# Kernel optimization log

Measured on AMD Instinct MI355X. Metric: run time of the kernel, lower is better.

## Reference

```python
import jax, jax.numpy as jnp
import numpy as np

WS = 16       # window size
SHIFT = 8     # shift size
HEADS = 16
DIM = 512
HIDDEN = 2048
B, H, W = 8, 64, 64
EPS = 1e-5


def _rel_coords_table(ws):
    h = np.arange(-(ws - 1), ws, dtype=np.float32)
    t = np.stack(np.meshgrid(h, h, indexing='ij'), axis=-1)  # (2ws-1, 2ws-1, 2)
    t = t / (ws - 1) * 8.0
    t = np.sign(t) * np.log2(np.abs(t) + 1.0) / np.log2(8.0)
    return t.reshape(-1, 2)


def _rel_pos_index(ws):
    coords = np.stack(np.meshgrid(np.arange(ws), np.arange(ws), indexing='ij'))
    cf = coords.reshape(2, -1)                      # (2, N)
    rel = (cf[:, :, None] - cf[:, None, :]).transpose(1, 2, 0)  # (N, N, 2)
    rel[..., 0] += ws - 1
    rel[..., 1] += ws - 1
    rel[..., 0] *= 2 * ws - 1
    return rel.sum(-1)                              # (N, N)


def _attn_mask(h, w, ws, shift):
    img = np.zeros((h, w))
    cnt = 0
    for hs in (slice(0, -ws), slice(-ws, -shift), slice(-shift, None)):
        for wsl in (slice(0, -ws), slice(-ws, -shift), slice(-shift, None)):
            img[hs, wsl] = cnt
            cnt += 1
    mw = img.reshape(h // ws, ws, w // ws, ws).transpose(0, 2, 1, 3).reshape(-1, ws * ws)
    am = mw[:, None, :] - mw[:, :, None]            # (nW, N, N)
    return np.where(am != 0, -100.0, 0.0).astype(np.float32)


def _ln(x, g, b):
    m = x.mean(-1, keepdims=True)
    v = ((x - m) ** 2).mean(-1, keepdims=True)
    return (x - m) * jax.lax.rsqrt(v + EPS) * g + b


def setup_inputs() -> dict:
    key = jax.random.key(0)
    ks = jax.random.split(key, 16)
    s = 0.02
    return {
        'x': jax.random.normal(ks[0], (B, H, W, DIM), jnp.float32),
        'qkv_w': jax.random.normal(ks[1], (3 * DIM, DIM), jnp.float32) * s,
        'q_bias': jnp.zeros((DIM,), jnp.float32),
        'v_bias': jnp.zeros((DIM,), jnp.float32),
        'logit_scale': jnp.full((HEADS, 1, 1), np.log(10.0), jnp.float32),
        'cpb_w1': jax.random.normal(ks[2], (512, 2), jnp.float32) * s,
        'cpb_b1': jnp.zeros((512,), jnp.float32),
        'cpb_w2': jax.random.normal(ks[3], (HEADS, 512), jnp.float32) * s,
        'proj_w': jax.random.normal(ks[4], (DIM, DIM), jnp.float32) * s,
        'proj_b': jnp.zeros((DIM,), jnp.float32),
        'norm1_g': jnp.ones((DIM,), jnp.float32),
        'norm1_b': jnp.zeros((DIM,), jnp.float32),
        'norm2_g': jnp.ones((DIM,), jnp.float32),
        'norm2_b': jnp.zeros((DIM,), jnp.float32),
        'fc1_w': jax.random.normal(ks[5], (HIDDEN, DIM), jnp.float32) * s,
        'fc1_b': jnp.zeros((HIDDEN,), jnp.float32),
        'fc2_w': jax.random.normal(ks[6], (DIM, HIDDEN), jnp.float32) * s,
        'fc2_b': jnp.zeros((DIM,), jnp.float32),
    }


def reference(x, qkv_w, q_bias, v_bias, logit_scale, cpb_w1, cpb_b1, cpb_w2,
              proj_w, proj_b, norm1_g, norm1_b, norm2_g, norm2_b,
              fc1_w, fc1_b, fc2_w, fc2_b):
    b, h, w, c = x.shape
    N = WS * WS
    nW = (h // WS) * (w // WS)
    hd = c // HEADS

    # --- shifted window cosine attention ---
    shifted = jnp.roll(x, (-SHIFT, -SHIFT), axis=(1, 2))
    xw = shifted.reshape(b, h // WS, WS, w // WS, WS, c)
    xw = xw.transpose(0, 1, 3, 2, 4, 5).reshape(-1, N, c)  # (b*nW, N, C)

    bias = jnp.concatenate([q_bias, jnp.zeros_like(q_bias), v_bias])
    qkv = (xw @ qkv_w.T + bias).reshape(-1, N, 3, HEADS, hd).transpose(2, 0, 3, 1, 4)
    q, k, v = qkv[0], qkv[1], qkv[2]  # (Bn, heads, N, hd)

    qn = q / jnp.maximum(jnp.linalg.norm(q, axis=-1, keepdims=True), 1e-12)
    kn = k / jnp.maximum(jnp.linalg.norm(k, axis=-1, keepdims=True), 1e-12)
    scale = jnp.exp(jnp.minimum(logit_scale, jnp.log(jnp.float32(100.0))))  # (heads,1,1)
    attn = jnp.einsum('bhnd,bhmd->bhnm', qn, kn) * scale

    # continuous relative position bias (CPB MLP)
    table = jnp.asarray(_rel_coords_table(WS))                    # (M, 2)
    t = jax.nn.relu(table @ cpb_w1.T + cpb_b1) @ cpb_w2.T          # (M, heads)
    idx = _rel_pos_index(WS).reshape(-1)
    rpb = t[idx].reshape(N, N, HEADS).transpose(2, 0, 1)
    rpb = 16.0 * jax.nn.sigmoid(rpb)
    attn = attn + rpb[None]

    mask = jnp.asarray(_attn_mask(h, w, WS, SHIFT))                # (nW, N, N)
    attn = attn.reshape(b, nW, HEADS, N, N) + mask[None, :, None]
    attn = jax.nn.softmax(attn.reshape(-1, HEADS, N, N), axis=-1)

    out = jnp.einsum('bhnm,bhmd->bhnd', attn, v).transpose(0, 2, 1, 3).reshape(-1, N, c)
    out = out @ proj_w.T + proj_b

    out = out.reshape(b, h // WS, w // WS, WS, WS, c)
    out = out.transpose(0, 1, 3, 2, 4, 5).reshape(b, h, w, c)
    out = jnp.roll(out, (SHIFT, SHIFT), axis=(1, 2))

    # post-norm residuals (SwinV2 style)
    x = x + _ln(out, norm1_g, norm1_b)
    hmid = jax.nn.gelu(x @ fc1_w.T + fc1_b, approximate=False)
    mlp_out = hmid @ fc2_w.T + fc2_b
    x = x + _ln(mlp_out, norm2_g, norm2_b)
    return x
```

## Files before the change

kernel.cpp:

```cpp
#include <hip/hip_runtime.h>
#include <math.h>


#define HEADS 16
#define HD 32
#define NTOK 256
#define DIMC 512
#define HIDDEN 2048

typedef __attribute__((ext_vector_type(8))) short bf16x8;
typedef __attribute__((ext_vector_type(4))) float f32x4;
typedef __attribute__((ext_vector_type(8))) unsigned short ushort8;

#define MFMA16(a, b, c) __builtin_amdgcn_mfma_f32_16x16x32_bf16((a), (b), (c), 0, 0, 0)
#define WAIT_VM(N) asm volatile("s_waitcnt vmcnt(" #N ")" ::: "memory")
#define WAIT_LGKM0 asm volatile("s_waitcnt lgkmcnt(0)" ::: "memory")

__device__ __forceinline__ unsigned short f2bf(float f) {
  union { float f; unsigned u; } v; v.f = f;
  unsigned r = v.u + 0x7FFFu + ((v.u >> 16) & 1u);
  return (unsigned short)(r >> 16);
}
__device__ __forceinline__ float bf2f(unsigned short h) {
  union { unsigned u; float f; } v; v.u = ((unsigned)h) << 16; return v.f;
}
__device__ __forceinline__ void gload16(const void* g, void* l) {
  __builtin_amdgcn_global_load_lds(
      (const __attribute__((address_space(1))) unsigned int*)g,
      (__attribute__((address_space(3))) unsigned int*)l, 16, 0, 0);
}
__device__ __forceinline__ bf16x8 ds_read128(const unsigned short* p) {
  unsigned off = (unsigned)(size_t)(const __attribute__((address_space(3))) unsigned short*)p;
  bf16x8 r;
  asm volatile("ds_read_b128 %0, %1" : "=v"(r) : "v"(off));
  return r;
}
__device__ __forceinline__ int band(int x) { return x < 48 ? 0 : (x < 56 ? 1 : 2); }

__device__ __forceinline__ float gelu_fast(float x) {
  float u2 = x * (1.5957691216f + 0.0713548163f * x * x);
  u2 = fminf(u2, 80.f);
  float e = __expf(u2);
  return x * (e / (e + 1.f));
}

__device__ __forceinline__ void gemm256_main(const unsigned short* Ab, const unsigned short* Bb,
                                             int K, unsigned short* aT, unsigned short* bT,
                                             f32x4 (&acc)[8][4]) {
  const int tid = threadIdx.x;
  const int w = tid >> 6, lane = tid & 63;
  const int cl = lane & 15, g = lane >> 4;
  const int wr = (w >> 2) * 128, wc = (w & 3) * 64;
  const int off0 = (2 * w) * 1024 + lane * 16;
  const int off1 = (2 * w + 1) * 1024 + lane * 16;
  const int r0 = off0 >> 6, c0 = ((off0 >> 4) & 3) ^ ((r0 >> 1) & 3);
  const int r1 = off1 >> 6, c1 = ((off1 >> 4) & 3) ^ ((r1 >> 1) & 3);
  const char* Ac = (const char*)Ab;
  const char* Bc = (const char*)Bb;
  const size_t sA0 = (size_t)r0 * (K * 2) + (size_t)c0 * 16;
  const size_t sA1 = (size_t)r1 * (K * 2) + (size_t)c1 * 16;
  const int T = K >> 5;
  int offB[4], offA0[4], offA1[4];
#pragma unroll
  for (int i = 0; i < 4; i++) {
    int rowb = wc + i * 16 + cl;
    offB[i] = rowb * 32 + ((g ^ ((rowb >> 1) & 3)) * 8);
    int rowa = wr + i * 16 + cl;
    offA0[i] = rowa * 32 + ((g ^ ((rowa >> 1) & 3)) * 8);
    int rowa1 = wr + 64 + i * 16 + cl;
    offA1[i] = rowa1 * 32 + ((g ^ ((rowa1 >> 1) & 3)) * 8);
  }
#pragma unroll
  for (int p = 0; p < 3; p++) {
    size_t kb = (size_t)p * 64;
    int bo = p * 16384;
    gload16(Ac + sA0 + kb, (char*)aT + bo + off0);
    gload16(Ac + sA1 + kb, (char*)aT + bo + off1);
    gload16(Bc + sA0 + kb, (char*)bT + bo + off0);
    gload16(Bc + sA1 + kb, (char*)bT + bo + off1);
  }
  WAIT_VM(8);
  __builtin_amdgcn_s_barrier();
  bf16x8 bfv[4], af[4];
#pragma unroll
  for (int ni = 0; ni < 4; ni++) bfv[ni] = ds_read128(bT + offB[ni]);
#pragma unroll
  for (int mi = 0; mi < 4; mi++) af[mi] = ds_read128(aT + offA0[mi]);

  for (int t = 0; t < T; t++) {
    const int cur = (t & 3) * 8192;
    if (t + 3 < T) {
      size_t kb = (size_t)(t + 3) * 64;
      int bo = ((t + 3) & 3) * 16384;
      gload16(Ac + sA0 + kb, (char*)aT + bo + off0);
      gload16(Ac + sA1 + kb, (char*)aT + bo + off1);
    }
    WAIT_LGKM0;
    __builtin_amdgcn_sched_barrier(0);
    __builtin_amdgcn_s_setprio(1);
#pragma unroll
    for (int mi = 0; mi < 4; mi++)
#pragma unroll
      for (int ni = 0; ni < 4; ni++) acc[mi][ni] = MFMA16(af[mi], bfv[ni], acc[mi][ni]);
    __builtin_amdgcn_s_setprio(0);
    bf16x8 af2[4];
#pragma unroll
    for (int mi = 0; mi < 4; mi++) af2[mi] = ds_read128(aT + cur + offA1[mi]);
    if (t + 3 < T) {
      size_t kb = (size_t)(t + 3) * 64;
      int bo = ((t + 3) & 3) * 16384;
      gload16(Bc + sA0 + kb, (char*)bT + bo + off0);
      gload16(Bc + sA1 + kb, (char*)bT + bo + off1);
    }
    WAIT_LGKM0;
    __builtin_amdgcn_sched_barrier(0);
    __builtin_amdgcn_s_setprio(1);
#pragma unroll
    for (int mi = 0; mi < 4; mi++)
#pragma unroll
      for (int ni = 0; ni < 4; ni++) acc[4 + mi][ni] = MFMA16(af2[mi], bfv[ni], acc[4 + mi][ni]);
    __builtin_amdgcn_s_setprio(0);
    if (t + 1 < T) {
      if (t + 3 < T) WAIT_VM(8);
      else if (t + 2 < T) WAIT_VM(4);
      else WAIT_VM(0);
      __builtin_amdgcn_s_barrier();
      const int nxt = ((t + 1) & 3) * 8192;
#pragma unroll
      for (int ni = 0; ni < 4; ni++) bfv[ni] = ds_read128(bT + nxt + offB[ni]);
#pragma unroll
      for (int mi = 0; mi < 4; mi++) af[mi] = ds_read128(aT + nxt + offA0[mi]);
    }
  }
}

__device__ __forceinline__ void xcd_swizzle(int& bm, int& bn) {
  int gy = gridDim.y;
  int nwg = gridDim.x * gy;
  int flat = blockIdx.y * gridDim.x + blockIdx.x;
  int cpx = nwg >> 3;
  int swz = (flat & 7) * cpx + (flat >> 3);
  bm = swz / gy;
  bn = swz % gy;
}

__global__ __launch_bounds__(512, 2) void gemm_qkv(const unsigned short* A,
                                                   const unsigned short* Bw, const float* qbias,
                                                   const float* vbias, unsigned short* qo,
                                                   unsigned short* ko, unsigned short* vo) {
  __shared__ unsigned short aT[4 * 8192];
  __shared__ unsigned short bT[4 * 8192];
  int bm, bn;
  xcd_swizzle(bm, bn);
  f32x4 acc[8][4] = {};
  gemm256_main(A + (size_t)bm * 256 * DIMC, Bw + (size_t)bn * 256 * DIMC, DIMC, aT, bT, acc);
  int lane = threadIdx.x & 63, w = threadIdx.x >> 6;
  int wr = (w >> 2) * 128, wc = (w & 3) * 64, g = lane >> 4, cl = lane & 15;
  int which = bn >> 1;
  unsigned short* base = which == 0 ? qo : (which == 1 ? ko : vo);
#pragma unroll
  for (int ni = 0; ni < 4; ni++) {
    int gn = bn * 256 + wc + ni * 16 + cl;
    int wn = gn & 511, head = wn >> 5, hd = wn & 31;
    float bv = (which == 0) ? qbias[wn] : (which == 2 ? vbias[wn] : 0.f);
#pragma unroll
    for (int mi = 0; mi < 8; mi++) {
#pragma unroll
      for (int reg = 0; reg < 4; reg++) {
        int gm = bm * 256 + wr + mi * 16 + 4 * g + reg;
        int win = gm >> 8, tok = gm & 255;
        base[(((size_t)(win * HEADS + head)) * NTOK + tok) * HD + hd] =
            f2bf(acc[mi][ni][reg] + bv);
      }
    }
  }
}

template <int GELU>
__global__ __launch_bounds__(512, 2) void gemm_epi(const unsigned short* A,
                                                   const unsigned short* Bw, const float* bias,
                                                   unsigned short* out, int N, int K) {
  __shared__ unsigned short aT[4 * 8192];
  __shared__ unsigned short bT[4 * 8192];
  int bm, bn;
  xcd_swizzle(bm, bn);
  f32x4 acc[8][4] = {};
  gemm256_main(A + (size_t)bm * 256 * K, Bw + (size_t)bn * 256 * K, K, aT, bT, acc);
  int lane = threadIdx.x & 63, w = threadIdx.x >> 6;
  int wr = (w >> 2) * 128, wc = (w & 3) * 64, g = lane >> 4, cl = lane & 15;
  float bv[4];
#pragma unroll
  for (int ni = 0; ni < 4; ni++) bv[ni] = bias[bn * 256 + wc + ni * 16 + cl];
#pragma unroll
  for (int mi = 0; mi < 8; mi++) {
#pragma unroll
    for (int reg = 0; reg < 4; reg++) {
      int gm = bm * 256 + wr + mi * 16 + 4 * g + reg;
      unsigned short* rowp = out + (size_t)gm * N + bn * 256 + wc + cl;
#pragma unroll
      for (int ni = 0; ni < 4; ni++) {
        float val = acc[mi][ni][reg] + bv[ni];
        if (GELU) val = gelu_fast(val);
        rowp[ni * 16] = f2bf(val);
      }
    }
  }
}

__global__ __launch_bounds__(256) void attn_kernel(const unsigned short* qg,
                                                   const unsigned short* kg,
                                                   const unsigned short* vg, const float* rpbt,
                                                   const float* logit_scale,
                                                   unsigned short* attn_out) {
  __shared__ unsigned short kS[256 * 32];
  __shared__ unsigned short vT[32 * 256];
  __shared__ unsigned short pS[64 * 256];

  int bid = blockIdx.x;
  int qb = bid & 3, h = (bid >> 2) & 15, win = bid >> 6;
  int tid = threadIdx.x, lane = tid & 63, w = tid >> 6;
  int g = lane >> 4, cl = lane & 15;
  const size_t whbase = ((size_t)(win * HEADS + h)) * NTOK * HD;
  const unsigned short* qwin = qg + whbase + (size_t)qb * 64 * HD;
  const unsigned short* kwin = kg + whbase;
  const unsigned short* vwin = vg + whbase;

#pragma unroll
  for (int i = 0; i < 4; i++) {
    int ci = i * 256 + tid, row = ci >> 2, gc = ci & 3;
    uint4 d = *(const uint4*)(kwin + row * 32 + gc * 8);
    *(uint4*)(kS + row * 32 + ((gc ^ ((row >> 1) & 3)) * 8)) = d;
  }
  {
    int tok = tid;
    ushort8 t0 = *(const ushort8*)(vwin + tok * 32);
    ushort8 t1 = *(const ushort8*)(vwin + tok * 32 + 8);
    ushort8 t2 = *(const ushort8*)(vwin + tok * 32 + 16);
    ushort8 t3 = *(const ushort8*)(vwin + tok * 32 + 24);
    int kc = tok >> 3, ki = tok & 7;
#pragma unroll
    for (int j = 0; j < 8; j++) {
      vT[(j)*256 + ((kc ^ (j & 7)) << 3) + ki] = t0[j];
      vT[(8 + j) * 256 + ((kc ^ ((8 + j) & 7)) << 3) + ki] = t1[j];
      vT[(16 + j) * 256 + ((kc ^ ((16 + j) & 7)) << 3) + ki] = t2[j];
      vT[(24 + j) * 256 + ((kc ^ ((24 + j) & 7)) << 3) + ki] = t3[j];
    }
  }
  __syncthreads();

  float scale = __expf(fminf(logit_scale[h], 4.6051702f));

  {
    int row = tid;
    int sw = (row >> 1) & 3;
    ushort8 ch[4];
#pragma unroll
    for (int gc = 0; gc < 4; gc++) ch[gc] = *(const ushort8*)(kS + row * 32 + ((gc ^ sw) * 8));
    float ss = 0.f;
#pragma unroll
    for (int gc = 0; gc < 4; gc++)
#pragma unroll
      for (int j = 0; j < 8; j++) { float f = bf2f(ch[gc][j]); ss += f * f; }
    float rn = rsqrtf(fmaxf(ss, 1e-24f));
#pragma unroll
    for (int gc = 0; gc < 4; gc++) {
      ushort8 o;
#pragma unroll
      for (int j = 0; j < 8; j++) o[j] = f2bf(bf2f(ch[gc][j]) * rn);
      *(ushort8*)(kS + row * 32 + ((gc ^ sw) * 8)) = o;
    }
  }

  bf16x8 qf;
  {
    int qrow = 16 * w + cl;
    ushort8 qraw = *(const ushort8*)(qwin + qrow * 32 + 8 * g);
    float qe[8];
    float ss = 0.f;
#pragma unroll
    for (int j = 0; j < 8; j++) { qe[j] = bf2f(qraw[j]); ss += qe[j] * qe[j]; }
    ss += __shfl_xor(ss, 16, 64);
    ss += __shfl_xor(ss, 32, 64);
    float rn = rsqrtf(fmaxf(ss, 1e-24f)) * scale;
#pragma unroll
    for (int j = 0; j < 8; j++) qf[j] = (short)f2bf(qe[j] * rn);
  }
  __syncthreads();

  f32x4 acc[16];
#pragma unroll
  for (int ct = 0; ct < 16; ct++) {
    int kr = ct * 16 + cl;
    bf16x8 kf = *(const bf16x8*)(kS + kr * 32 + ((g ^ ((kr >> 1) & 3)) * 8));
    f32x4 z = {0.f, 0.f, 0.f, 0.f};
    acc[ct] = MFMA16(qf, kf, z);
  }

  int wh = (win >> 2) & 3, ww = win & 3;
  int bandcc = band(ww * 16 + cl);
  const float* rpbh = rpbt + h * 961;
  float m4[4];
  int baseidx[4], ridq[4];
#pragma unroll
  for (int reg = 0; reg < 4; reg++) {
    int qrow = qb * 64 + 16 * w + 4 * g + reg;
    int ri = qrow >> 4, ci = qrow & 15;
    ridq[reg] = 3 * band(wh * 16 + ri) + band(ww * 16 + ci);
    baseidx[reg] = (ri + 15) * 31 + (ci + 15 - cl);
    m4[reg] = -1e30f;
  }
#pragma unroll
  for (int ct = 0; ct < 16; ct++) {
    int brc = 3 * band(wh * 16 + ct);
#pragma unroll
    for (int reg = 0; reg < 4; reg++) {
      float v = acc[ct][reg] + rpbh[baseidx[reg] - ct * 31] +
                ((ridq[reg] != (brc + bandcc)) ? -100.f : 0.f);
      acc[ct][reg] = v;
      m4[reg] = fmaxf(m4[reg], v);
    }
  }
#pragma unroll
  for (int reg = 0; reg < 4; reg++) {
#pragma unroll
    for (int o = 1; o < 16; o <<= 1) m4[reg] = fmaxf(m4[reg], __shfl_xor(m4[reg], o, 64));
  }

  float s4[4] = {0.f, 0.f, 0.f, 0.f};
#pragma unroll
  for (int ct = 0; ct < 16; ct++) {
#pragma unroll
    for (int reg = 0; reg < 4; reg++) {
      float p = __expf(acc[ct][reg] - m4[reg]);
      s4[reg] += p;
      int row = 16 * w + 4 * g + reg;
      int c = ct * 16 + cl;
      pS[row * 256 + (((c >> 3) ^ (row & 7)) << 3) + (c & 7)] = f2bf(p);
    }
  }
#pragma unroll
  for (int reg = 0; reg < 4; reg++) {
#pragma unroll
    for (int o = 1; o < 16; o <<= 1) s4[reg] += __shfl_xor(s4[reg], o, 64);
  }

  f32x4 o0 = {0.f, 0.f, 0.f, 0.f}, o1 = {0.f, 0.f, 0.f, 0.f};
  int prow = 16 * w + cl;
#pragma unroll
  for (int ks = 0; ks < 8; ks++) {
    bf16x8 pf = *(const bf16x8*)(pS + prow * 256 + ((((ks * 4 + g)) ^ (prow & 7)) << 3));
    int kc = ks * 4 + g;
    bf16x8 vf0 = *(const bf16x8*)(vT + cl * 256 + ((kc ^ (cl & 7)) << 3));
    bf16x8 vf1 = *(const bf16x8*)(vT + (16 + cl) * 256 + ((kc ^ ((16 + cl) & 7)) << 3));
    o0 = MFMA16(pf, vf0, o0);
    o1 = MFMA16(pf, vf1, o1);
  }

#pragma unroll
  for (int reg = 0; reg < 4; reg++) {
    int row = 16 * w + 4 * g + reg;
    float linv = 1.f / s4[reg];
    size_t tokg = (size_t)win * NTOK + qb * 64 + row;
    attn_out[tokg * DIMC + h * 32 + cl] = f2bf(o0[reg] * linv);
    attn_out[tokg * DIMC + h * 32 + 16 + cl] = f2bf(o1[reg] * linv);
  }
}

__global__ __launch_bounds__(256) void cvt_bf16(const float* src, unsigned short* dst, int n8) {
  int i = blockIdx.x * 256 + threadIdx.x;
  if (i >= n8) return;
  const float* s = src + (size_t)i * 8;
  float4 a = *(const float4*)s, b = *(const float4*)(s + 4);
  ushort8 o;
  o[0] = f2bf(a.x); o[1] = f2bf(a.y); o[2] = f2bf(a.z); o[3] = f2bf(a.w);
  o[4] = f2bf(b.x); o[5] = f2bf(b.y); o[6] = f2bf(b.z); o[7] = f2bf(b.w);
  *(ushort8*)(dst + (size_t)i * 8) = o;
}

__device__ __forceinline__ float cpb_coord(int i) {
  float t = (float)(i - 15) * (8.f / 15.f);
  float s = (t > 0.f) ? 1.f : ((t < 0.f) ? -1.f : 0.f);
  return s * log2f(fabsf(t) + 1.f) * (1.f / 3.f);
}

__global__ __launch_bounds__(256) void cpb_kernel(const float* w1, const float* b1, const float* w2,
                                                  float* rpbt) {
  int i = blockIdx.x * 256 + threadIdx.x;
  if (i >= 961 * 16) return;
  int m = i >> 4, h = i & 15;
  int mi = m / 31, mj = m % 31;
  float c0 = cpb_coord(mi), c1 = cpb_coord(mj);
  float acc = 0.f;
  for (int j = 0; j < 512; j++) {
    float hv = fmaxf(w1[2 * j] * c0 + w1[2 * j + 1] * c1 + b1[j], 0.f);
    acc += hv * w2[h * 512 + j];
  }
  rpbt[h * 961 + m] = 16.f / (1.f + __expf(-acc));
}

__global__ __launch_bounds__(256) void xw_gather(const float* x, unsigned short* xw) {
  int idx = blockIdx.x * 256 + threadIdx.x;
  int m = idx >> 6, chunk = idx & 63;
  int win = m >> 8, tok = m & 255;
  int b = win >> 4, wh = (win >> 2) & 3, ww = win & 3;
  int tr = tok >> 4, tc = tok & 15;
  int sr = (wh * 16 + tr + 8) & 63, sc = (ww * 16 + tc + 8) & 63;
  const float* src = x + ((size_t)((b * 64 + sr) * 64 + sc)) * 512 + chunk * 8;
  float4 a = *(const float4*)src, bq = *(const float4*)(src + 4);
  ushort8 o;
  o[0] = f2bf(a.x); o[1] = f2bf(a.y); o[2] = f2bf(a.z); o[3] = f2bf(a.w);
  o[4] = f2bf(bq.x); o[5] = f2bf(bq.y); o[6] = f2bf(bq.z); o[7] = f2bf(bq.w);
  *(ushort8*)(xw + (size_t)m * 512 + chunk * 8) = o;
}

__global__ __launch_bounds__(256) void ln1_kernel(const unsigned short* pr, const float* x,
                                                  const float* gw, const float* bw,
                                                  unsigned short* x1b) {
  int w = threadIdx.x >> 6, lane = threadIdx.x & 63;
  size_t t = (size_t)blockIdx.x * 4 + w;
  int ti = (int)t;
  int b = ti >> 12, rc = ti & 4095, r = rc >> 6, c = rc & 63;
  int sr = (r + 56) & 63, sc = (c + 56) & 63;
  int win = b * 16 + (sr >> 4) * 4 + (sc >> 4);
  int tok = (sr & 15) * 16 + (sc & 15);
  int ch = lane * 8;
  ushort8 pv = *(const ushort8*)(pr + ((size_t)win * 256 + tok) * 512 + ch);
  float pf[8];
  float s = 0.f, s2 = 0.f;
#pragma unroll
  for (int j = 0; j < 8; j++) { pf[j] = bf2f(pv[j]); s += pf[j]; s2 += pf[j] * pf[j]; }
#pragma unroll
  for (int o = 1; o < 64; o <<= 1) { s += __shfl_xor(s, o, 64); s2 += __shfl_xor(s2, o, 64); }
  float mean = s * (1.f / 512.f);
  float rstd = rsqrtf(s2 * (1.f / 512.f) - mean * mean + 1e-5f);
  const float* xrow = x + t * 512 + ch;
  float4 xa = *(const float4*)xrow, xb = *(const float4*)(xrow + 4);
  float xs[8] = {xa.x, xa.y, xa.z, xa.w, xb.x, xb.y, xb.z, xb.w};
  ushort8 o8;
#pragma unroll
  for (int j = 0; j < 8; j++) {
    float y = (pf[j] - mean) * rstd * gw[ch + j] + bw[ch + j];
    o8[j] = f2bf(xs[j] + y);
  }
  *(ushort8*)(x1b + t * 512 + ch) = o8;
}

__global__ __launch_bounds__(256) void ln2_kernel(const unsigned short* mp,
                                                  const unsigned short* x1b, const float* gw,
                                                  const float* bw, float* out) {
  int w = threadIdx.x >> 6, lane = threadIdx.x & 63;
  size_t t = (size_t)blockIdx.x * 4 + w;
  int ch = lane * 8;
  ushort8 mv = *(const ushort8*)(mp + t * 512 + ch);
  float pf[8];
  float s = 0.f, s2 = 0.f;
#pragma unroll
  for (int j = 0; j < 8; j++) { pf[j] = bf2f(mv[j]); s += pf[j]; s2 += pf[j] * pf[j]; }
#pragma unroll
  for (int o = 1; o < 64; o <<= 1) { s += __shfl_xor(s, o, 64); s2 += __shfl_xor(s2, o, 64); }
  float mean = s * (1.f / 512.f);
  float rstd = rsqrtf(s2 * (1.f / 512.f) - mean * mean + 1e-5f);
  ushort8 xv = *(const ushort8*)(x1b + t * 512 + ch);
  float vals[8];
#pragma unroll
  for (int j = 0; j < 8; j++)
    vals[j] = bf2f(xv[j]) + (pf[j] - mean) * rstd * gw[ch + j] + bw[ch + j];
  *(float4*)(out + t * 512 + ch) = make_float4(vals[0], vals[1], vals[2], vals[3]);
  *(float4*)(out + t * 512 + ch + 4) = make_float4(vals[4], vals[5], vals[6], vals[7]);
}

extern "C" void kernel_launch(void* const* d_in, const int* in_sizes, int n_in, void* d_out,
                              int out_size, void* d_ws, size_t ws_size, hipStream_t stream) {
  (void)in_sizes; (void)n_in; (void)out_size; (void)ws_size;
  const float* x = (const float*)d_in[0];
  const float* qkv_w = (const float*)d_in[1];
  const float* q_bias = (const float*)d_in[2];
  const float* v_bias = (const float*)d_in[3];
  const float* logit_sc = (const float*)d_in[4];
  const float* cpb_w1 = (const float*)d_in[5];
  const float* cpb_b1 = (const float*)d_in[6];
  const float* cpb_w2 = (const float*)d_in[7];
  const float* proj_w = (const float*)d_in[8];
  const float* proj_b = (const float*)d_in[9];
  const float* n1g = (const float*)d_in[10];
  const float* n1b = (const float*)d_in[11];
  const float* n2g = (const float*)d_in[12];
  const float* n2b = (const float*)d_in[13];
  const float* fc1_w = (const float*)d_in[14];
  const float* fc1_b = (const float*)d_in[15];
  const float* fc2_w = (const float*)d_in[16];
  const float* fc2_b = (const float*)d_in[17];

  char* ws = (char*)d_ws;
  unsigned short* wq = (unsigned short*)(ws);
  unsigned short* wp = (unsigned short*)(ws + (2ll << 20));
  unsigned short* w1 = (unsigned short*)(ws + (4ll << 20));
  unsigned short* w2 = (unsigned short*)(ws + (8ll << 20));
  float* rpbt = (float*)(ws + (12ll << 20));
  unsigned short* xw = (unsigned short*)(ws + (16ll << 20));
  unsigned short* qbuf = (unsigned short*)(ws + (48ll << 20));
  unsigned short* kbuf = (unsigned short*)(ws + (80ll << 20));
  unsigned short* vbuf = (unsigned short*)(ws + (112ll << 20));
  unsigned short* projout = (unsigned short*)(ws + (144ll << 20));
  unsigned short* x1b = (unsigned short*)(ws + (176ll << 20));
  unsigned short* hmid = (unsigned short*)(ws + (48ll << 20));
  unsigned short* mlpout = xw;
  float* out = (float*)d_out;

  cvt_bf16<<<dim3(384), dim3(256), 0, stream>>>(qkv_w, wq, 1536 * 512 / 8);
  cvt_bf16<<<dim3(128), dim3(256), 0, stream>>>(proj_w, wp, 512 * 512 / 8);
  cvt_bf16<<<dim3(512), dim3(256), 0, stream>>>(fc1_w, w1, 2048 * 512 / 8);
  cvt_bf16<<<dim3(512), dim3(256), 0, stream>>>(fc2_w, w2, 512 * 2048 / 8);
  cpb_kernel<<<dim3(61), dim3(256), 0, stream>>>(cpb_w1, cpb_b1, cpb_w2, rpbt);
  xw_gather<<<dim3(8192), dim3(256), 0, stream>>>(x, xw);

  gemm_qkv<<<dim3(128, 6), dim3(512), 0, stream>>>(xw, wq, q_bias, v_bias, qbuf, kbuf, vbuf);
  attn_kernel<<<dim3(8192), dim3(256), 0, stream>>>(qbuf, kbuf, vbuf, rpbt, logit_sc, xw);
  gemm_epi<0><<<dim3(128, 2), dim3(512), 0, stream>>>(xw, wp, proj_b, projout, 512, 512);
  ln1_kernel<<<dim3(8192), dim3(256), 0, stream>>>(projout, x, n1g, n1b, x1b);

  gemm_epi<1><<<dim3(128, 8), dim3(512), 0, stream>>>(x1b, w1, fc1_b, hmid, 2048, 512);
  gemm_epi<0><<<dim3(128, 2), dim3(512), 0, stream>>>(hmid, w2, fc2_b, mlpout, 512, 2048);
  ln2_kernel<<<dim3(8192), dim3(256), 0, stream>>>(mlpout, x1b, n2g, n2b, out);
}
```

Baseline: 476.1 us.

## Use double-buffered GEMM pipeline and drop softmax max pass with constant bound

The GEMM main loop goes from a 4-stage, 3-ahead prefetch pipeline to a 2-stage double buffer, halving LDS per block and waiting for all global loads each iteration. In attention, the row-max reduction and its shuffles are removed; the exponent subtracts a constant upper bound (scale + 16) instead, since cosine similarity times scale plus at most 16 bias bounds every logit. The smaller LDS footprint may allow more resident blocks, at the cost of less latency hiding in the GEMMs. The constant-bound softmax stays correct only while the logits remain within exp range.

```diff
diff --git a/kernel.cpp b/kernel.cpp
--- a/kernel.cpp
+++ b/kernel.cpp
@@ -70,16 +70,11 @@
     int rowa1 = wr + 64 + i * 16 + cl;
     offA1[i] = rowa1 * 32 + ((g ^ ((rowa1 >> 1) & 3)) * 8);
   }
-#pragma unroll
-  for (int p = 0; p < 3; p++) {
-    size_t kb = (size_t)p * 64;
-    int bo = p * 16384;
-    gload16(Ac + sA0 + kb, (char*)aT + bo + off0);
-    gload16(Ac + sA1 + kb, (char*)aT + bo + off1);
-    gload16(Bc + sA0 + kb, (char*)bT + bo + off0);
-    gload16(Bc + sA1 + kb, (char*)bT + bo + off1);
-  }
-  WAIT_VM(8);
+  gload16(Ac + sA0, (char*)aT + off0);
+  gload16(Ac + sA1, (char*)aT + off1);
+  gload16(Bc + sA0, (char*)bT + off0);
+  gload16(Bc + sA1, (char*)bT + off1);
+  WAIT_VM(0);
   __builtin_amdgcn_s_barrier();
   bf16x8 bfv[4], af[4];
 #pragma unroll
@@ -88,12 +83,13 @@
   for (int mi = 0; mi < 4; mi++) af[mi] = ds_read128(aT + offA0[mi]);
 
   for (int t = 0; t < T; t++) {
-    const int cur = (t & 3) * 8192;
-    if (t + 3 < T) {
-      size_t kb = (size_t)(t + 3) * 64;
-      int bo = ((t + 3) & 3) * 16384;
-      gload16(Ac + sA0 + kb, (char*)aT + bo + off0);
-      gload16(Ac + sA1 + kb, (char*)aT + bo + off1);
+    const int cur = (t & 1) * 8192, nxt = 8192 - cur;
+    if (t + 1 < T) {
+      size_t kb = (size_t)(t + 1) * 64;
+      gload16(Ac + sA0 + kb, (char*)aT + nxt * 2 + off0);
+      gload16(Ac + sA1 + kb, (char*)aT + nxt * 2 + off1);
+      gload16(Bc + sA0 + kb, (char*)bT + nxt * 2 + off0);
+      gload16(Bc + sA1 + kb, (char*)bT + nxt * 2 + off1);
     }
     WAIT_LGKM0;
     __builtin_amdgcn_sched_barrier(0);
@@ -106,12 +102,6 @@
     bf16x8 af2[4];
 #pragma unroll
     for (int mi = 0; mi < 4; mi++) af2[mi] = ds_read128(aT + cur + offA1[mi]);
-    if (t + 3 < T) {
-      size_t kb = (size_t)(t + 3) * 64;
-      int bo = ((t + 3) & 3) * 16384;
-      gload16(Bc + sA0 + kb, (char*)bT + bo + off0);
-      gload16(Bc + sA1 + kb, (char*)bT + bo + off1);
-    }
     WAIT_LGKM0;
     __builtin_amdgcn_sched_barrier(0);
     __builtin_amdgcn_s_setprio(1);
@@ -121,11 +111,8 @@
       for (int ni = 0; ni < 4; ni++) acc[4 + mi][ni] = MFMA16(af2[mi], bfv[ni], acc[4 + mi][ni]);
     __builtin_amdgcn_s_setprio(0);
     if (t + 1 < T) {
-      if (t + 3 < T) WAIT_VM(8);
-      else if (t + 2 < T) WAIT_VM(4);
-      else WAIT_VM(0);
+      WAIT_VM(0);
       __builtin_amdgcn_s_barrier();
-      const int nxt = ((t + 1) & 3) * 8192;
 #pragma unroll
       for (int ni = 0; ni < 4; ni++) bfv[ni] = ds_read128(bT + nxt + offB[ni]);
 #pragma unroll
@@ -148,8 +135,8 @@
                                                    const unsigned short* Bw, const float* qbias,
                                                    const float* vbias, unsigned short* qo,
                                                    unsigned short* ko, unsigned short* vo) {
-  __shared__ unsigned short aT[4 * 8192];
-  __shared__ unsigned short bT[4 * 8192];
+  __shared__ unsigned short aT[2 * 8192];
+  __shared__ unsigned short bT[2 * 8192];
   int bm, bn;
   xcd_swizzle(bm, bn);
   f32x4 acc[8][4] = {};
@@ -180,8 +167,8 @@
 __global__ __launch_bounds__(512, 2) void gemm_epi(const unsigned short* A,
                                                    const unsigned short* Bw, const float* bias,
                                                    unsigned short* out, int N, int K) {
-  __shared__ unsigned short aT[4 * 8192];
-  __shared__ unsigned short bT[4 * 8192];
+  __shared__ unsigned short aT[2 * 8192];
+  __shared__ unsigned short bT[2 * 8192];
   int bm, bn;
   xcd_swizzle(bm, bn);
   f32x4 acc[8][4] = {};
@@ -299,7 +286,7 @@
   int wh = (win >> 2) & 3, ww = win & 3;
   int bandcc = band(ww * 16 + cl);
   const float* rpbh = rpbt + h * 961;
-  float m4[4];
+  const float C = scale + 16.f;
   int baseidx[4], ridq[4];
 #pragma unroll
   for (int reg = 0; reg < 4; reg++) {
@@ -307,8 +294,8 @@
     int ri = qrow >> 4, ci = qrow & 15;
     ridq[reg] = 3 * band(wh * 16 + ri) + band(ww * 16 + ci);
     baseidx[reg] = (ri + 15) * 31 + (ci + 15 - cl);
-    m4[reg] = -1e30f;
-  }
+  }
+  float s4[4] = {0.f, 0.f, 0.f, 0.f};
 #pragma unroll
   for (int ct = 0; ct < 16; ct++) {
     int brc = 3 * band(wh * 16 + ct);
@@ -316,22 +303,7 @@
     for (int reg = 0; reg < 4; reg++) {
       float v = acc[ct][reg] + rpbh[baseidx[reg] - ct * 31] +
                 ((ridq[reg] != (brc + bandcc)) ? -100.f : 0.f);
-      acc[ct][reg] = v;
-      m4[reg] = fmaxf(m4[reg], v);
-    }
-  }
-#pragma unroll
-  for (int reg = 0; reg < 4; reg++) {
-#pragma unroll
-    for (int o = 1; o < 16; o <<= 1) m4[reg] = fmaxf(m4[reg], __shfl_xor(m4[reg], o, 64));
-  }
-
-  float s4[4] = {0.f, 0.f, 0.f, 0.f};
-#pragma unroll
-  for (int ct = 0; ct < 16; ct++) {
-#pragma unroll
-    for (int reg = 0; reg < 4; reg++) {
-      float p = __expf(acc[ct][reg] - m4[reg]);
+      float p = __expf(v - C);
       s4[reg] += p;
       int row = 16 * w + 4 * g + reg;
       int c = ct * 16 + cl;
```

Result: slower. 499.7 us (+4.9%).
